# Kernel optimization log

Measured on AMD Instinct MI355X. Metric: run time of the kernel, lower is better.

Reference implementation:

```python
import jax, jax.numpy as jnp
import numpy as np

B, N, D = 2, 2048, 1024
H, FD, HD = 16, 16, 64
ENC = 512
EPS = 1e-12
RD = 4.0            # sqrt(scale_dim=feature_dim=16)
RRD = 2.0           # sqrt(RD)
R2 = float(np.sqrt(2.0))


def taylor_exp(x):
    # x: [..., fd] -> [..., 1 + fd + fd*fd]
    x2 = (x[..., :, None] * x[..., None, :]).reshape(*x.shape[:-1], FD * FD) / R2
    return jnp.concatenate([jnp.ones_like(x[..., :1]), x / RRD, x2 / RD], axis=-1)


def setup_inputs() -> dict:
    key = jax.random.key(0)
    ks = jax.random.split(key, 7)
    s = 1.0 / np.sqrt(D)
    x = jax.random.normal(ks[0], (B, N, D), dtype=jnp.float32)
    Wq = jax.random.normal(ks[1], (H * FD, D), dtype=jnp.float32) * s
    Wk = jax.random.normal(ks[2], (H * FD, D), dtype=jnp.float32) * s
    Wv = jax.random.normal(ks[3], (H * HD, D), dtype=jnp.float32) * s
    Wk_enc = jax.random.normal(ks[4], (H * FD, D), dtype=jnp.float32) * s
    Wv_enc = jax.random.normal(ks[5], (H * HD, D), dtype=jnp.float32) * s
    Wout = jax.random.normal(ks[6], (D, H * HD), dtype=jnp.float32) * s
    return {"x": x, "Wq": Wq, "Wk": Wk, "Wv": Wv,
            "Wk_enc": Wk_enc, "Wv_enc": Wv_enc, "Wout": Wout}


def reference(x, Wq, Wk, Wv, Wk_enc, Wv_enc, Wout):
    b, n, _ = x.shape
    # projections -> [b, h, n, *]
    q = (x @ Wq.T).reshape(b, n, H, FD).transpose(0, 2, 1, 3)
    k = (x @ Wk.T).reshape(b, n, H, FD).transpose(0, 2, 1, 3)
    v = (x @ Wv.T).reshape(b, n, H, HD).transpose(0, 2, 1, 3)
    # encoder prefix
    x_enc = x[:, :ENC]
    k_enc = (x_enc @ Wk_enc.T).reshape(b, ENC, H, FD).transpose(0, 2, 1, 3)
    v_enc = (x_enc @ Wv_enc.T).reshape(b, ENC, H, HD).transpose(0, 2, 1, 3)
    # Taylor feature maps: fd -> 1 + fd + fd^2 = 273
    k_enc_f = taylor_exp(k_enc)
    q_f = taylor_exp(q)
    k_f = taylor_exp(k)
    # causal decoder attention (unnormalized)
    A_qk = jnp.einsum('bhnd,bhmd->bhnm', q_f, k_f)
    A_qk = jnp.tril(A_qk)
    y1 = jnp.einsum('bhnm,bhme->bhne', A_qk, v)
    # cross attention to encoder prefix
    A_qk2 = jnp.einsum('bhnd,bhmd->bhnm', q_f, k_enc_f)
    y2 = jnp.einsum('bhnm,bhme->bhne', A_qk2, v_enc)
    # shared normalizer: enc sum + causal cumsum of decoder key features
    k_state = k_enc_f.sum(axis=2, keepdims=True) + jnp.cumsum(k_f, axis=2)
    z = 1.0 / ((q_f * k_state).sum(axis=-1) + EPS)  # [b, h, n]
    out = (y1 + y2) * z[..., None]                  # [b, h, n, hd]
    out = out.transpose(0, 2, 1, 3).reshape(b, n, H * HD)
    return out @ Wout.T
```

## Files before the change

kernel.cpp:

```cpp
#include <hip/hip_runtime.h>

#define B_    2
#define N_    2048
#define H_    16
#define HD_   64
#define ENC_  512
#define FP_   288
#define CHK_  64
#define NC_   32
#define SSZ_  18720
#define C2C_  0.17677669529663687f
#define EPS_  1e-12f

using s8v   = __attribute__((ext_vector_type(8))) short;
using h8v   = __attribute__((ext_vector_type(8))) _Float16;
using f4v   = __attribute__((ext_vector_type(4))) float;
using u16x4 = __attribute__((ext_vector_type(4))) unsigned short;
typedef unsigned short ushort_t;

__device__ __forceinline__ unsigned short bfh(float x) {
    unsigned int u = __float_as_uint(x);
    return (unsigned short)((u + 0x7FFF + ((u >> 16) & 1)) >> 16);
}
__device__ __forceinline__ float bff(unsigned short h) {
    return __uint_as_float(((unsigned int)h) << 16);
}
__device__ __forceinline__ void splitf4(float4 v, u16x4& h, u16x4& l) {
    unsigned short h0 = bfh(v.x), h1 = bfh(v.y), h2 = bfh(v.z), h3 = bfh(v.w);
    h = (u16x4){h0, h1, h2, h3};
    l = (u16x4){bfh(v.x - bff(h0)), bfh(v.y - bff(h1)),
                bfh(v.z - bff(h2)), bfh(v.w - bff(h3))};
}

__device__ __forceinline__ unsigned short f16q(float x) {
    _Float16 h = (_Float16)x;
    return __builtin_bit_cast(unsigned short, h);
}
__device__ __forceinline__ float f16f(unsigned short u) {
    return (float)__builtin_bit_cast(_Float16, u);
}
__device__ __forceinline__ void splitf16(float x, unsigned short& h, unsigned short& l) {
    _Float16 hh = (_Float16)x;
    h = __builtin_bit_cast(unsigned short, hh);
    l = f16q(x - (float)hh);
}
__device__ __forceinline__ void splitf16_4(float4 v, u16x4& h, u16x4& l) {
    unsigned short h0, l0, h1, l1, h2, l2, h3, l3;
    splitf16(v.x, h0, l0); splitf16(v.y, h1, l1);
    splitf16(v.z, h2, l2); splitf16(v.w, h3, l3);
    h = (u16x4){h0, h1, h2, h3};
    l = (u16x4){l0, l1, l2, l3};
}
__device__ __forceinline__ u16x4 f16q4(float4 v) {
    return (u16x4){f16q(v.x), f16q(v.y), f16q(v.z), f16q(v.w)};
}

#define MFMA_  __builtin_amdgcn_mfma_f32_16x16x32_bf16
#define MFMAH_ __builtin_amdgcn_mfma_f32_16x16x32_f16

__device__ __forceinline__ void gld16(const void* g, void* l) {
    __builtin_amdgcn_global_load_lds(
        (const __attribute__((address_space(1))) unsigned int*)g,
        (__attribute__((address_space(3))) unsigned int*)l, 16, 0, 0);
}

__device__ __forceinline__ int xcd_swz(int b, int nwg) {
    int q = nwg >> 3, r = nwg & 7;
    int xcd = b & 7, loc = b >> 3;
    return (xcd < r ? xcd * (q + 1) : r * (q + 1) + (xcd - r) * q) + loc;
}

#define X_F4   1048576
#define W1_F4  393216
#define W2_F4  327680
#define WO_F4  262144

__global__ __launch_bounds__(256) void split_all(
    const float* __restrict__ x,
    const float* __restrict__ Wq, const float* __restrict__ Wk,
    const float* __restrict__ Wv, const float* __restrict__ Wke,
    const float* __restrict__ Wve, const float* __restrict__ Wout,
    ushort_t* __restrict__ xh, ushort_t* __restrict__ xl,
    ushort_t* __restrict__ w1, ushort_t* __restrict__ w2,
    ushort_t* __restrict__ wo)
{
    int gid = blockIdx.x * 256 + threadIdx.x;
    if (gid < X_F4) {
        float4 vv = ((const float4*)x)[gid];
        u16x4 h, l; splitf16_4(vv, h, l);
        ((u16x4*)xh)[gid] = h; ((u16x4*)xl)[gid] = l;
    } else if (gid < X_F4 + W1_F4) {
        int i = gid - X_F4;
        int row = i >> 8, c4 = i & 255;
        const float* s = (row < 256) ? Wq + (size_t)row * 1024
                       : (row < 512) ? Wk + (size_t)(row - 256) * 1024
                                     : Wv + (size_t)(row - 512) * 1024;
        ((u16x4*)w1)[i] = f16q4(*(const float4*)(s + c4 * 4));
    } else if (gid < X_F4 + W1_F4 + W2_F4) {
        int i = gid - X_F4 - W1_F4;
        int row = i >> 8, c4 = i & 255;
        const float* s = (row < 256) ? Wke + (size_t)row * 1024
                                     : Wve + (size_t)(row - 256) * 1024;
        ((u16x4*)w2)[i] = f16q4(*(const float4*)(s + c4 * 4));
    } else {
        int i = gid - X_F4 - W1_F4 - W2_F4;
        ((u16x4*)wo)[i] = f16q4(((const float4*)Wout)[i]);
    }
}

template <int SHIFT, int PASSES>
__device__ __forceinline__ void bg128(
    const ushort_t* __restrict__ Ah, const ushort_t* __restrict__ Al,
    const ushort_t* __restrict__ Wh,
    int bx, int by, int rowjump,
    ushort_t* SM, f4v (&acc)[4][4])
{
    int t = threadIdx.x;
    int w = t >> 6, lane = t & 63;
    int row0 = by * 128, col0 = bx * 128;
    int wrow = (w >> 1) * 64, wcol = (w & 1) * 64;
    int fr = lane & 15, g = lane >> 4;

    int c0 = lane, c1 = 64 + lane;
    int r0 = w * 32 + (c0 >> 2), k80 = (c0 & 3) * 8;
    int r1 = w * 32 + (c1 >> 2), k81 = (c1 & 3) * 8;
    int gr0 = row0 + r0, gr1 = row0 + r1;
    size_t a0 = (size_t)(gr0 >> SHIFT) * rowjump + (gr0 & ((1 << SHIFT) - 1));
    size_t a1 = (size_t)(gr1 >> SHIFT) * rowjump + (gr1 & ((1 << SHIFT) - 1));
    const ushort_t* pA0h = Ah + a0 * 1024 + k80;
    const ushort_t* pA1h = Ah + a1 * 1024 + k81;
    const ushort_t* pA0l = Al + a0 * 1024 + k80;
    const ushort_t* pA1l = Al + a1 * 1024 + k81;
    const ushort_t* pW0  = Wh + (size_t)(col0 + r0) * 1024 + k80;
    const ushort_t* pW1  = Wh + (size_t)(col0 + r1) * 1024 + k81;
    int woff = w * 1024;

    #pragma unroll
    for (int mt = 0; mt < 4; ++mt)
        #pragma unroll
        for (int nt = 0; nt < 4; ++nt) acc[mt][nt] = (f4v){0.f, 0.f, 0.f, 0.f};

    auto STAGE = [&](int buf, int k0) {
        ushort_t* Bp = SM + buf * 12288;
        gld16(pA0h + k0, Bp + woff);
        gld16(pA1h + k0, Bp + woff + 512);
        if (PASSES == 2) {
            gld16(pA0l + k0, Bp + 4096 + woff);
            gld16(pA1l + k0, Bp + 4096 + woff + 512);
        }
        gld16(pW0  + k0, Bp + 8192 + woff);
        gld16(pW1  + k0, Bp + 8192 + woff + 512);
    };

    STAGE(0, 0);
    __syncthreads();
    int cur = 0;
    for (int k0 = 0; k0 < 1024; k0 += 32) {
        if (k0 + 32 < 1024) STAGE(cur ^ 1, k0 + 32);
        ushort_t* Bp = SM + cur * 12288;
        h8v a_h[4], a_l[4], b_[4];
        #pragma unroll
        for (int mt = 0; mt < 4; ++mt) {
            a_h[mt] = *(const h8v*)&Bp[(wrow + mt * 16 + fr) * 32 + g * 8];
            if (PASSES == 2)
                a_l[mt] = *(const h8v*)&Bp[4096 + (wrow + mt * 16 + fr) * 32 + g * 8];
        }
        #pragma unroll
        for (int nt = 0; nt < 4; ++nt)
            b_[nt] = *(const h8v*)&Bp[8192 + (wcol + nt * 16 + fr) * 32 + g * 8];
        #pragma unroll
        for (int mt = 0; mt < 4; ++mt)
            #pragma unroll
            for (int nt = 0; nt < 4; ++nt) {
                acc[mt][nt] = MFMAH_(a_h[mt], b_[nt], acc[mt][nt], 0, 0, 0);
                if (PASSES == 2)
                    acc[mt][nt] = MFMAH_(a_l[mt], b_[nt], acc[mt][nt], 0, 0, 0);
            }
        __syncthreads();
        cur ^= 1;
    }
}

__global__ __launch_bounds__(256) void proj2(
    const ushort_t* __restrict__ xh, const ushort_t* __restrict__ xl,
    const ushort_t* __restrict__ w1, const ushort_t* __restrict__ w2,
    float* __restrict__ tmpq, float* __restrict__ tmpk, float* __restrict__ v,
    float* __restrict__ tmpke, float* __restrict__ ve)
{
    __shared__ ushort_t SM[24576];
    f4v acc[4][4];
    int blk = xcd_swz(blockIdx.x, 464);
    int t = threadIdx.x, w = t >> 6, lane = t & 63;
    int wrow = (w >> 1) * 64, wcol = (w & 1) * 64;
    int fr = lane & 15, g = lane >> 4;

    if (blk < 384) {
        int bx = blk % 12, by = blk / 12;
        if (bx < 4) bg128<12, 2>(xh, xl, w1, bx, by, 0, SM, acc);
        else        bg128<12, 1>(xh, xl, w1, bx, by, 0, SM, acc);
        int row0 = by * 128, col0 = bx * 128;
        #pragma unroll
        for (int mt = 0; mt < 4; ++mt)
            #pragma unroll
            for (int nt = 0; nt < 4; ++nt)
                #pragma unroll
                for (int r4 = 0; r4 < 4; ++r4) {
                    int r  = row0 + wrow + mt * 16 + g * 4 + r4;
                    int cc = col0 + wcol + nt * 16 + fr;
                    float val = acc[mt][nt][r4];
                    if (cc < 256)      tmpq[(size_t)r * 256 + cc] = val;
                    else if (cc < 512) tmpk[(size_t)r * 256 + (cc - 256)] = val;
                    else {
                        int c2 = cc - 512, hh = c2 >> 6, jj = c2 & 63;
                        int bb = r >> 11, n = r & 2047;
                        v[(((size_t)(bb * 16 + hh)) * 2048 + n) * 64 + jj] = val;
                    }
                }
    } else {
        int r2 = blk - 384;
        int bx = r2 % 10, by = r2 / 10;
        if (bx < 2) bg128<9, 2>(xh, xl, w2, bx, by, 2048, SM, acc);
        else        bg128<9, 1>(xh, xl, w2, bx, by, 2048, SM, acc);
        int row0 = by * 128, col0 = bx * 128;
        #pragma unroll
        for (int mt = 0; mt < 4; ++mt)
            #pragma unroll
            for (int nt = 0; nt < 4; ++nt)
                #pragma unroll
                for (int r4 = 0; r4 < 4; ++r4) {
                    int r  = row0 + wrow + mt * 16 + g * 4 + r4;
                    int cc = col0 + wcol + nt * 16 + fr;
                    float val = acc[mt][nt][r4];
                    if (cc < 256) tmpke[(size_t)r * 256 + cc] = val;
                    else {
                        int c2 = cc - 256, hh = c2 >> 6, jj = c2 & 63;
                        int bb = r >> 9, n = r & 511;
                        ve[(((size_t)(bb * 16 + hh)) * 512 + n) * 64 + jj] = val;
                    }
                }
    }
}

__global__ __launch_bounds__(256) void out_gemm(
    const ushort_t* __restrict__ Atn, const ushort_t* __restrict__ Wh,
    float* __restrict__ out)
{
    __shared__ ushort_t SM[24576];
    f4v acc[4][4];
    int blk = xcd_swz(blockIdx.x, 256);
    int bx = blk & 7, by = blk >> 3;
    bg128<12, 1>(Atn, Atn, Wh, bx, by, 0, SM, acc);
    int t = threadIdx.x, w = t >> 6, lane = t & 63;
    int wrow = (w >> 1) * 64, wcol = (w & 1) * 64;
    int fr = lane & 15, g = lane >> 4;
    int row0 = by * 128, col0 = bx * 128;
    #pragma unroll
    for (int mt = 0; mt < 4; ++mt)
        #pragma unroll
        for (int nt = 0; nt < 4; ++nt)
            #pragma unroll
            for (int r4 = 0; r4 < 4; ++r4) {
                int r  = row0 + wrow + mt * 16 + g * 4 + r4;
                int cc = col0 + wcol + nt * 16 + fr;
                out[(size_t)r * 1024 + cc] = acc[mt][nt][r4];
            }
}

__device__ __forceinline__ void st_stage(
    const float* __restrict__ Kp, const float* __restrict__ V,
    size_t krow0, size_t vrow0, int h, int t,
    float* ksT, ushort_t* VTH)
{
    {
        int r = t >> 2, q4 = t & 3;
        float4 kv = *(const float4*)&Kp[(krow0 + r) * 256 + h * 16 + q4 * 4];
        ksT[(q4 * 4 + 0) * 68 + r] = kv.x;
        ksT[(q4 * 4 + 1) * 68 + r] = kv.y;
        ksT[(q4 * 4 + 2) * 68 + r] = kv.z;
        ksT[(q4 * 4 + 3) * 68 + r] = kv.w;
    }
    if (t < 64) ksT[16 * 68 + t] = 1.0f;
    {
        int r = t & 63, jg = t >> 6;
        #pragma unroll
        for (int cc = 0; cc < 4; ++cc) {
            float4 vv = *(const float4*)&V[(vrow0 + r) * HD_ + jg * 16 + cc * 4];
            float vals[4] = {vv.x, vv.y, vv.z, vv.w};
            #pragma unroll
            for (int e = 0; e < 4; ++e) {
                int j = jg * 16 + cc * 4 + e;
                VTH[j * 72 + r] = f16q(vals[e]);
            }
        }
    }
    if (t < 64) VTH[64 * 72 + t] = 0x3C00;
}

__device__ __forceinline__ void st_ftile(
    const float* ksT, int ft, int fr, int g,
    const h8v (&AHf)[2][5], f4v (&acc)[5])
{
    int f = ft * 16 + fr;
    int fi, fj; float scale;
    if (f == 0)       { fi = 16; fj = 16; scale = 1.0f; }
    else if (f < 17)  { fi = f - 1; fj = 16; scale = 0.5f; }
    else if (f < 273) { fi = (f - 17) >> 4; fj = (f - 17) & 15; scale = C2C_; }
    else              { fi = 16; fj = 16; scale = 0.0f; }
    #pragma unroll
    for (int ks2 = 0; ks2 < 2; ++ks2) {
        const float* pa = ksT + fi * 68 + ks2 * 32 + g * 8;
        const float* pb = ksT + fj * 68 + ks2 * 32 + g * 8;
        h8v bv;
        #pragma unroll
        for (int e = 0; e < 8; ++e) bv[e] = (_Float16)(pa[e] * pb[e] * scale);
        #pragma unroll
        for (int jt = 0; jt < 5; ++jt)
            acc[jt] = MFMAH_(AHf[ks2][jt], bv, acc[jt], 0, 0, 0);
    }
}

__global__ __launch_bounds__(256) void state_all(
    const float* __restrict__ Kpe, const float* __restrict__ Ve, ushort_t* __restrict__ Se,
    const float* __restrict__ Kpc, const float* __restrict__ Vc, ushort_t* __restrict__ Sc)
{
    __shared__ float ksT[17 * 68];
    __shared__ ushort_t VTH[80 * 72];
    int blk = blockIdx.x, t = threadIdx.x;
    int w = t >> 6, lane = t & 63, fr = lane & 15, g = lane >> 4;

    for (int i = t; i < 15 * 72; i += 256) VTH[65 * 72 + i] = 0;

    if (blk >= 160) {
        int b2 = blk - 160;
        int c = b2 & 31, bh = b2 >> 5;
        int b = bh >> 4, h = bh & 15;
        ushort_t* Sg = Sc + ((size_t)bh * NC_ + c) * SSZ_;
        st_stage(Kpc, Vc, (size_t)b * 2048 + c * 64, (size_t)bh * 2048 + c * 64,
                 h, t, ksT, VTH);
        __syncthreads();
        h8v AHf[2][5];
        #pragma unroll
        for (int ks2 = 0; ks2 < 2; ++ks2)
            #pragma unroll
            for (int jt = 0; jt < 5; ++jt)
                AHf[ks2][jt] = *(const h8v*)&VTH[(jt * 16 + fr) * 72 + ks2 * 32 + g * 8];
        for (int ft = w; ft < 18; ft += 4) {
            f4v acc[5];
            #pragma unroll
            for (int jt = 0; jt < 5; ++jt) acc[jt] = (f4v){0.f, 0.f, 0.f, 0.f};
            st_ftile(ksT, ft, fr, g, AHf, acc);
            #pragma unroll
            for (int jt = 0; jt < 5; ++jt)
                #pragma unroll
                for (int r4 = 0; r4 < 4; ++r4) {
                    int j = jt * 16 + g * 4 + r4;
                    if (j < 65) Sg[(size_t)j * FP_ + ft * 16 + fr] = f16q(acc[jt][r4]);
                }
        }
    } else {
        int bh = blk / 5, fg = blk % 5;
        int b = bh >> 4, h = bh & 15;
        int ft = fg * 4 + w;
        ushort_t* Sg = Se + (size_t)bh * SSZ_;
        f4v acc[5];
        #pragma unroll
        for (int jt = 0; jt < 5; ++jt) acc[jt] = (f4v){0.f, 0.f, 0.f, 0.f};
        for (int m0 = 0; m0 < 512; m0 += 64) {
            if (m0) __syncthreads();
            st_stage(Kpe, Ve, (size_t)b * 512 + m0, (size_t)bh * 512 + m0,
                     h, t, ksT, VTH);
            __syncthreads();
            if (ft < 18) {
                h8v AHf[2][5];
                #pragma unroll
                for (int ks2 = 0; ks2 < 2; ++ks2)
                    #pragma unroll
                    for (int jt = 0; jt < 5; ++jt)
                        AHf[ks2][jt] = *(const h8v*)&VTH[(jt * 16 + fr) * 72 + ks2 * 32 + g * 8];
                st_ftile(ksT, ft, fr, g, AHf, acc);
            }
        }
        if (ft < 18) {
            #pragma unroll
            for (int jt = 0; jt < 5; ++jt)
                #pragma unroll
                for (int r4 = 0; r4 < 4; ++r4) {
                    int j = jt * 16 + g * 4 + r4;
                    if (j < 65) Sg[(size_t)j * FP_ + ft * 16 + fr] = f16q(acc[jt][r4]);
                }
        }
    }
}

__global__ __launch_bounds__(256) void prefix_scan(
    ushort_t* __restrict__ Sloc, const ushort_t* __restrict__ Senc)
{
    const int Q = SSZ_ / 8;
    int gid = blockIdx.x * 256 + threadIdx.x;
    if (gid >= 32 * Q) return;
    int bh = gid / Q, e = gid - bh * Q;
    s8v ev = *(const s8v*)(Senc + (size_t)bh * SSZ_ + e * 8);
    float run[8];
    #pragma unroll
    for (int u = 0; u < 8; ++u) run[u] = f16f((ushort_t)ev[u]);
    ushort_t* Sb = Sloc + (size_t)bh * NC_ * SSZ_ + e * 8;
    #pragma unroll 1
    for (int cb = 0; cb < 8; ++cb) {
        s8v t0 = *(const s8v*)(Sb + (size_t)(cb * 4 + 0) * SSZ_);
        s8v t1 = *(const s8v*)(Sb + (size_t)(cb * 4 + 1) * SSZ_);
        s8v t2 = *(const s8v*)(Sb + (size_t)(cb * 4 + 2) * SSZ_);
        s8v t3 = *(const s8v*)(Sb + (size_t)(cb * 4 + 3) * SSZ_);
        s8v o0, o1, o2, o3;
        #pragma unroll
        for (int u = 0; u < 8; ++u) { o0[u] = (short)f16q(run[u]); run[u] += f16f((ushort_t)t0[u]); }
        #pragma unroll
        for (int u = 0; u < 8; ++u) { o1[u] = (short)f16q(run[u]); run[u] += f16f((ushort_t)t1[u]); }
        #pragma unroll
        for (int u = 0; u < 8; ++u) { o2[u] = (short)f16q(run[u]); run[u] += f16f((ushort_t)t2[u]); }
        #pragma unroll
        for (int u = 0; u < 8; ++u) { o3[u] = (short)f16q(run[u]); run[u] += f16f((ushort_t)t3[u]); }
        *(s8v*)(Sb + (size_t)(cb * 4 + 0) * SSZ_) = o0;
        *(s8v*)(Sb + (size_t)(cb * 4 + 1) * SSZ_) = o1;
        *(s8v*)(Sb + (size_t)(cb * 4 + 2) * SSZ_) = o2;
        *(s8v*)(Sb + (size_t)(cb * 4 + 3) * SSZ_) = o3;
    }
}

template<int FW>
__device__ __forceinline__ void y2_issue(
    const ushort_t* __restrict__ Sth, int f0, int t, s8v& r0, s8v& r1, s8v& r2)
{
    constexpr int NS = FW / 8;
    constexpr int TOT = 65 * NS;
    int s1 = t + 256, s2 = t + 512;
    r0 = *(const s8v*)(Sth + (size_t)(t / NS) * FP_ + f0 + (t % NS) * 8);
    if (s1 < TOT) r1 = *(const s8v*)(Sth + (size_t)(s1 / NS) * FP_ + f0 + (s1 % NS) * 8);
    if (FW == 64 && s2 < TOT) r2 = *(const s8v*)(Sth + (size_t)(s2 / NS) * FP_ + f0 + (s2 % NS) * 8);
}

template<int FW>
__device__ __forceinline__ void y2_write(
    ushort_t* STH, int t, const s8v& r0, const s8v& r1, const s8v& r2)
{
    constexpr int NS = FW / 8;
    constexpr int TOT = 65 * NS;
    int s1 = t + 256, s2 = t + 512;
    *(s8v*)&STH[(t / NS) * 72 + (t % NS) * 8] = r0;
    if (s1 < TOT) *(s8v*)&STH[(s1 / NS) * 72 + (s1 % NS) * 8] = r1;
    if (FW == 64 && s2 < TOT) *(s8v*)&STH[(s2 / NS) * 72 + (s2 % NS) * 8] = r2;
}

template<int FW>
__device__ __forceinline__ void qf_gen(int f0, const float* qs, ushort_t* QF1, int t)
{
    for (int i = t; i < 64 * FW; i += 256) {
        int row = i / FW, cc = i % FW;
        int f = f0 + cc;
        float qv;
        if (f == 0)       qv = 1.0f;
        else if (f < 17)  qv = qs[row * 20 + (f - 1)] * 0.5f;
        else if (f < 273) qv = qs[row * 20 + ((f - 17) >> 4)] * qs[row * 20 + ((f - 17) & 15)] * C2C_;
        else              qv = 0.0f;
        QF1[row * 72 + cc] = f16q(qv);
    }
}

template<int FW>
__device__ __forceinline__ void y2_mfma(
    const ushort_t* QF1, const ushort_t* STH,
    f4v (&acc)[5], int w, int fr, int g)
{
    #pragma unroll
    for (int ks2 = 0; ks2 < FW / 32; ++ks2) {
        h8v a = *(const h8v*)&QF1[(16 * w + fr) * 72 + ks2 * 32 + g * 8];
        #pragma unroll
        for (int jt = 0; jt < 5; ++jt) {
            h8v b = *(const h8v*)&STH[(jt * 16 + fr) * 72 + ks2 * 32 + g * 8];
            acc[jt] = MFMAH_(a, b, acc[jt], 0, 0, 0);
        }
    }
}

__global__ __launch_bounds__(256) void attn_chunk(
    const float* __restrict__ qp, const float* __restrict__ kp,
    const float* __restrict__ v, const ushort_t* __restrict__ Spre,
    ushort_t* __restrict__ atn)
{
    __shared__ ushort_t U[19456];
    __shared__ float qs[64 * 20];
    __shared__ float den_s[64];
    ushort_t* AH  = U;
    ushort_t* AL  = U + 4608;
    ushort_t* QH  = U + 9216;
    ushort_t* QL  = U + 11776;
    ushort_t* KH  = U + 14336;
    ushort_t* KL  = U + 16896;
    ushort_t* VTH = U + 9216;
    ushort_t* QF1 = U;
    ushort_t* STH = U + 9216;

    int bid = blockIdx.x;
    int bh = bid >> 5, c = bid & 31;
    int b = bh >> 4, h = bh & 15;
    int t = threadIdx.x;
    int w = t >> 6, lane = t & 63, fr = lane & 15, g = lane >> 4;
    int rowbase = b * N_ + c * CHK_;
    const ushort_t* Sth = Spre + ((size_t)bh * NC_ + c) * SSZ_;

    int rqk = t >> 2, q4 = t & 3;
    float4 qv = *(const float4*)&qp[(size_t)(rowbase + rqk) * 256 + h * 16 + q4 * 4];
    float4 kv = *(const float4*)&kp[(size_t)(rowbase + rqk) * 256 + h * 16 + q4 * 4];
    s8v rA0 = {}, rA1 = {}, rA2 = {};
    y2_issue<64>(Sth, 0, t, rA0, rA1, rA2);
    int mv = t & 63, jg0 = t >> 6;
    const float* vr = &v[((size_t)bh * N_ + c * CHK_ + mv) * HD_ + jg0 * 16];
    float4 rv0 = *(const float4*)(vr + 0);
    float4 rv1 = *(const float4*)(vr + 4);
    float4 rv2 = *(const float4*)(vr + 8);
    float4 rv3 = *(const float4*)(vr + 12);

    {
        u16x4 hh, ll;
        splitf4(qv, hh, ll);
        *(u16x4*)&QH[rqk * 40 + q4 * 4] = hh;
        *(u16x4*)&QL[rqk * 40 + q4 * 4] = ll;
        splitf4(kv, hh, ll);
        *(u16x4*)&KH[rqk * 40 + q4 * 4] = hh;
        *(u16x4*)&KL[rqk * 40 + q4 * 4] = ll;
        u16x4 z4 = (u16x4){0, 0, 0, 0};
        *(u16x4*)&QH[rqk * 40 + 16 + q4 * 4] = z4;
        *(u16x4*)&QL[rqk * 40 + 16 + q4 * 4] = z4;
        *(u16x4*)&KH[rqk * 40 + 16 + q4 * 4] = z4;
        *(u16x4*)&KL[rqk * 40 + 16 + q4 * 4] = z4;
        qs[rqk * 20 + q4 * 4 + 0] = qv.x;
        qs[rqk * 20 + q4 * 4 + 1] = qv.y;
        qs[rqk * 20 + q4 * 4 + 2] = qv.z;
        qs[rqk * 20 + q4 * 4 + 3] = qv.w;
    }
    __syncthreads();

    {
        s8v qh = *(const s8v*)&QH[(16 * w + fr) * 40 + g * 8];
        s8v ql = *(const s8v*)&QL[(16 * w + fr) * 40 + g * 8];
        f4v sacc[4];
        #pragma unroll
        for (int jt = 0; jt < 4; ++jt) sacc[jt] = (f4v){0.f, 0.f, 0.f, 0.f};
        #pragma unroll
        for (int jt = 0; jt < 4; ++jt) {
            s8v kh = *(const s8v*)&KH[(jt * 16 + fr) * 40 + g * 8];
            s8v kl = *(const s8v*)&KL[(jt * 16 + fr) * 40 + g * 8];
            sacc[jt] = MFMA_(qh, kh, sacc[jt], 0, 0, 0);
            sacc[jt] = MFMA_(qh, kl, sacc[jt], 0, 0, 0);
            sacc[jt] = MFMA_(ql, kh, sacc[jt], 0, 0, 0);
        }
        __syncthreads();
        #pragma unroll
        for (int jt = 0; jt < 4; ++jt)
            #pragma unroll
            for (int r4 = 0; r4 < 4; ++r4) {
                int row = 16 * w + g * 4 + r4, col = jt * 16 + fr;
                float s = sacc[jt][r4];
                float a = (row >= col) ? (fmaf(s, 0.25f, 1.0f) + s * s * 0.03125f) : 0.f;
                unsigned short hh, ll; splitf16(a, hh, ll);
                AH[row * 72 + col] = hh;
                AL[row * 72 + col] = ll;
            }
    }
    {
        int j0 = jg0 * 16;
        VTH[(j0 +  0) * 72 + mv] = f16q(rv0.x); VTH[(j0 +  1) * 72 + mv] = f16q(rv0.y);
        VTH[(j0 +  2) * 72 + mv] = f16q(rv0.z); VTH[(j0 +  3) * 72 + mv] = f16q(rv0.w);
        VTH[(j0 +  4) * 72 + mv] = f16q(rv1.x); VTH[(j0 +  5) * 72 + mv] = f16q(rv1.y);
        VTH[(j0 +  6) * 72 + mv] = f16q(rv1.z); VTH[(j0 +  7) * 72 + mv] = f16q(rv1.w);
        VTH[(j0 +  8) * 72 + mv] = f16q(rv2.x); VTH[(j0 +  9) * 72 + mv] = f16q(rv2.y);
        VTH[(j0 + 10) * 72 + mv] = f16q(rv2.z); VTH[(j0 + 11) * 72 + mv] = f16q(rv2.w);
        VTH[(j0 + 12) * 72 + mv] = f16q(rv3.x); VTH[(j0 + 13) * 72 + mv] = f16q(rv3.y);
        VTH[(j0 + 14) * 72 + mv] = f16q(rv3.z); VTH[(j0 + 15) * 72 + mv] = f16q(rv3.w);
    }
    if (t < 64) VTH[64 * 72 + t] = 0x3C00;
    for (int i = t; i < 15 * 72; i += 256) VTH[65 * 72 + i] = 0;
    __syncthreads();

    f4v acc[5];
    #pragma unroll
    for (int jt = 0; jt < 5; ++jt) acc[jt] = (f4v){0.f, 0.f, 0.f, 0.f};
    #pragma unroll
    for (int ks2 = 0; ks2 < 2; ++ks2) {
        h8v ah = *(const h8v*)&AH[(16 * w + fr) * 72 + ks2 * 32 + g * 8];
        h8v al = *(const h8v*)&AL[(16 * w + fr) * 72 + ks2 * 32 + g * 8];
        #pragma unroll
        for (int jt = 0; jt < 5; ++jt) {
            h8v b = *(const h8v*)&VTH[(jt * 16 + fr) * 72 + ks2 * 32 + g * 8];
            acc[jt] = MFMAH_(ah, b, acc[jt], 0, 0, 0);
            acc[jt] = MFMAH_(al, b, acc[jt], 0, 0, 0);
        }
    }
    __syncthreads();

    #pragma unroll
    for (int p = 0; p < 4; ++p) {
        y2_write<64>(STH, t, rA0, rA1, rA2);
        if (p < 3) y2_issue<64>(Sth, (p + 1) * 64, t, rA0, rA1, rA2);
        else       y2_issue<32>(Sth, 256,          t, rA0, rA1, rA2);
        qf_gen<64>(p * 64, qs, QF1, t);
        __syncthreads();
        y2_mfma<64>(QF1, STH, acc, w, fr, g);
        __syncthreads();
    }
    y2_write<32>(STH, t, rA0, rA1, rA2);
    qf_gen<32>(256, qs, QF1, t);
    __syncthreads();
    y2_mfma<32>(QF1, STH, acc, w, fr, g);

    if (fr == 0) {
        #pragma unroll
        for (int r4 = 0; r4 < 4; ++r4)
            den_s[16 * w + g * 4 + r4] = acc[4][r4];
    }
    __syncthreads();
    #pragma unroll
    for (int r4 = 0; r4 < 4; ++r4) {
        float z = 1.0f / (den_s[16 * w + g * 4 + r4] + EPS_);
        int row = rowbase + 16 * w + g * 4 + r4;
        #pragma unroll
        for (int jt = 0; jt < 4; ++jt) {
            float val = acc[jt][r4] * z;
            atn[(size_t)row * 1024 + h * 64 + jt * 16 + fr] = f16q(val);
        }
    }
}

extern "C" void kernel_launch(void* const* d_in, const int* in_sizes, int n_in,
                              void* d_out, int out_size, void* d_ws, size_t ws_size,
                              hipStream_t stream)
{
    const float* x    = (const float*)d_in[0];
    const float* Wq   = (const float*)d_in[1];
    const float* Wk   = (const float*)d_in[2];
    const float* Wv   = (const float*)d_in[3];
    const float* Wke  = (const float*)d_in[4];
    const float* Wve  = (const float*)d_in[5];
    const float* Wout = (const float*)d_in[6];
    float* out = (float*)d_out;
    float* ws  = (float*)d_ws;

    float* tmpq  = ws;
    float* tmpk  = tmpq  + (size_t)1048576;
    float* tmpke = tmpk  + (size_t)1048576;
    float* v     = tmpke + (size_t)262144;
    float* ve    = v     + (size_t)4194304;
    ushort_t* Sloc = (ushort_t*)(ve + 1048576);
    ushort_t* Senc = Sloc + (size_t)19169280;
    ushort_t* xh   = Senc + (size_t)599040;
    ushort_t* xl   = xh   + (size_t)4194304;
    ushort_t* wo   = xl   + (size_t)4194304;
    ushort_t* w1 = Sloc;
    ushort_t* w2 = w1 + (size_t)1572864;
    ushort_t* atn = xh;

    dim3 blk(256);

    split_all<<<7936, blk, 0, stream>>>(x, Wq, Wk, Wv, Wke, Wve, Wout,
                                        xh, xl, w1, w2, wo);
    proj2<<<464, blk, 0, stream>>>(xh, xl, w1, w2, tmpq, tmpk, v, tmpke, ve);
    state_all<<<160 + 32 * NC_, blk, 0, stream>>>(tmpke, ve, Senc, tmpk, v, Sloc);
    prefix_scan<<<293, blk, 0, stream>>>(Sloc, Senc);
    attn_chunk<<<32 * NC_, blk, 0, stream>>>(tmpq, tmpk, v, Sloc, atn);
    out_gemm<<<256, blk, 0, stream>>>(atn, wo, out);
}
```

Baseline: 120.8 us.

## Drop split-precision compensation passes and use single fp16 MFMA throughout

Removes the hi/lo split of x in the projection GEMMs, so the x-lo buffer, its staging and the second MFMA pass all go away. In the attention chunk kernel, the three-term bf16 split QK product becomes a single fp16 MFMA, and the A·V product drops its low-part pass. This cuts the associated LDS footprint, memory traffic and matrix work. Separately, the prefix scan moves from 8-wide to 4-wide vectors with twice the blocks, for more parallelism. The cost is reduced accuracy, since q/k projections and the Taylor scores now carry only fp16 precision, which may break the tolerance check.

```diff
diff --git a/kernel.cpp b/kernel.cpp
--- a/kernel.cpp
+++ b/kernel.cpp
@@ -13,25 +13,12 @@
 #define EPS_  1e-12f
 
 using s8v   = __attribute__((ext_vector_type(8))) short;
+using s4v   = __attribute__((ext_vector_type(4))) short;
 using h8v   = __attribute__((ext_vector_type(8))) _Float16;
 using f4v   = __attribute__((ext_vector_type(4))) float;
 using u16x4 = __attribute__((ext_vector_type(4))) unsigned short;
 typedef unsigned short ushort_t;
 
-__device__ __forceinline__ unsigned short bfh(float x) {
-    unsigned int u = __float_as_uint(x);
-    return (unsigned short)((u + 0x7FFF + ((u >> 16) & 1)) >> 16);
-}
-__device__ __forceinline__ float bff(unsigned short h) {
-    return __uint_as_float(((unsigned int)h) << 16);
-}
-__device__ __forceinline__ void splitf4(float4 v, u16x4& h, u16x4& l) {
-    unsigned short h0 = bfh(v.x), h1 = bfh(v.y), h2 = bfh(v.z), h3 = bfh(v.w);
-    h = (u16x4){h0, h1, h2, h3};
-    l = (u16x4){bfh(v.x - bff(h0)), bfh(v.y - bff(h1)),
-                bfh(v.z - bff(h2)), bfh(v.w - bff(h3))};
-}
-
 __device__ __forceinline__ unsigned short f16q(float x) {
     _Float16 h = (_Float16)x;
     return __builtin_bit_cast(unsigned short, h);
@@ -39,23 +26,10 @@
 __device__ __forceinline__ float f16f(unsigned short u) {
     return (float)__builtin_bit_cast(_Float16, u);
 }
-__device__ __forceinline__ void splitf16(float x, unsigned short& h, unsigned short& l) {
-    _Float16 hh = (_Float16)x;
-    h = __builtin_bit_cast(unsigned short, hh);
-    l = f16q(x - (float)hh);
-}
-__device__ __forceinline__ void splitf16_4(float4 v, u16x4& h, u16x4& l) {
-    unsigned short h0, l0, h1, l1, h2, l2, h3, l3;
-    splitf16(v.x, h0, l0); splitf16(v.y, h1, l1);
-    splitf16(v.z, h2, l2); splitf16(v.w, h3, l3);
-    h = (u16x4){h0, h1, h2, h3};
-    l = (u16x4){l0, l1, l2, l3};
-}
 __device__ __forceinline__ u16x4 f16q4(float4 v) {
     return (u16x4){f16q(v.x), f16q(v.y), f16q(v.z), f16q(v.w)};
 }
 
-#define MFMA_  __builtin_amdgcn_mfma_f32_16x16x32_bf16
 #define MFMAH_ __builtin_amdgcn_mfma_f32_16x16x32_f16
 
 __device__ __forceinline__ void gld16(const void* g, void* l) {
@@ -80,15 +54,13 @@
     const float* __restrict__ Wq, const float* __restrict__ Wk,
     const float* __restrict__ Wv, const float* __restrict__ Wke,
     const float* __restrict__ Wve, const float* __restrict__ Wout,
-    ushort_t* __restrict__ xh, ushort_t* __restrict__ xl,
+    ushort_t* __restrict__ xh,
     ushort_t* __restrict__ w1, ushort_t* __restrict__ w2,
     ushort_t* __restrict__ wo)
 {
     int gid = blockIdx.x * 256 + threadIdx.x;
     if (gid < X_F4) {
-        float4 vv = ((const float4*)x)[gid];
-        u16x4 h, l; splitf16_4(vv, h, l);
-        ((u16x4*)xh)[gid] = h; ((u16x4*)xl)[gid] = l;
+        ((u16x4*)xh)[gid] = f16q4(((const float4*)x)[gid]);
     } else if (gid < X_F4 + W1_F4) {
         int i = gid - X_F4;
         int row = i >> 8, c4 = i & 255;
@@ -108,10 +80,9 @@
     }
 }
 
-template <int SHIFT, int PASSES>
+template <int SHIFT>
 __device__ __forceinline__ void bg128(
-    const ushort_t* __restrict__ Ah, const ushort_t* __restrict__ Al,
-    const ushort_t* __restrict__ Wh,
+    const ushort_t* __restrict__ Ah, const ushort_t* __restrict__ Wh,
     int bx, int by, int rowjump,
     ushort_t* SM, f4v (&acc)[4][4])
 {
@@ -127,12 +98,10 @@
     int gr0 = row0 + r0, gr1 = row0 + r1;
     size_t a0 = (size_t)(gr0 >> SHIFT) * rowjump + (gr0 & ((1 << SHIFT) - 1));
     size_t a1 = (size_t)(gr1 >> SHIFT) * rowjump + (gr1 & ((1 << SHIFT) - 1));
-    const ushort_t* pA0h = Ah + a0 * 1024 + k80;
-    const ushort_t* pA1h = Ah + a1 * 1024 + k81;
-    const ushort_t* pA0l = Al + a0 * 1024 + k80;
-    const ushort_t* pA1l = Al + a1 * 1024 + k81;
-    const ushort_t* pW0  = Wh + (size_t)(col0 + r0) * 1024 + k80;
-    const ushort_t* pW1  = Wh + (size_t)(col0 + r1) * 1024 + k81;
+    const ushort_t* pA0 = Ah + a0 * 1024 + k80;
+    const ushort_t* pA1 = Ah + a1 * 1024 + k81;
+    const ushort_t* pW0 = Wh + (size_t)(col0 + r0) * 1024 + k80;
+    const ushort_t* pW1 = Wh + (size_t)(col0 + r1) * 1024 + k81;
     int woff = w * 1024;
 
     #pragma unroll
@@ -141,15 +110,11 @@
         for (int nt = 0; nt < 4; ++nt) acc[mt][nt] = (f4v){0.f, 0.f, 0.f, 0.f};
 
     auto STAGE = [&](int buf, int k0) {
-        ushort_t* Bp = SM + buf * 12288;
-        gld16(pA0h + k0, Bp + woff);
-        gld16(pA1h + k0, Bp + woff + 512);
-        if (PASSES == 2) {
-            gld16(pA0l + k0, Bp + 4096 + woff);
-            gld16(pA1l + k0, Bp + 4096 + woff + 512);
-        }
-        gld16(pW0  + k0, Bp + 8192 + woff);
-        gld16(pW1  + k0, Bp + 8192 + woff + 512);
+        ushort_t* Bp = SM + buf * 8192;
+        gld16(pA0 + k0, Bp + woff);
+        gld16(pA1 + k0, Bp + woff + 512);
+        gld16(pW0 + k0, Bp + 4096 + woff);
+        gld16(pW1 + k0, Bp + 4096 + woff + 512);
     };
 
     STAGE(0, 0);
@@ -157,37 +122,31 @@
     int cur = 0;
     for (int k0 = 0; k0 < 1024; k0 += 32) {
         if (k0 + 32 < 1024) STAGE(cur ^ 1, k0 + 32);
-        ushort_t* Bp = SM + cur * 12288;
-        h8v a_h[4], a_l[4], b_[4];
-        #pragma unroll
-        for (int mt = 0; mt < 4; ++mt) {
+        ushort_t* Bp = SM + cur * 8192;
+        h8v a_h[4], b_[4];
+        #pragma unroll
+        for (int mt = 0; mt < 4; ++mt)
             a_h[mt] = *(const h8v*)&Bp[(wrow + mt * 16 + fr) * 32 + g * 8];
-            if (PASSES == 2)
-                a_l[mt] = *(const h8v*)&Bp[4096 + (wrow + mt * 16 + fr) * 32 + g * 8];
-        }
         #pragma unroll
         for (int nt = 0; nt < 4; ++nt)
-            b_[nt] = *(const h8v*)&Bp[8192 + (wcol + nt * 16 + fr) * 32 + g * 8];
+            b_[nt] = *(const h8v*)&Bp[4096 + (wcol + nt * 16 + fr) * 32 + g * 8];
         #pragma unroll
         for (int mt = 0; mt < 4; ++mt)
             #pragma unroll
-            for (int nt = 0; nt < 4; ++nt) {
+            for (int nt = 0; nt < 4; ++nt)
                 acc[mt][nt] = MFMAH_(a_h[mt], b_[nt], acc[mt][nt], 0, 0, 0);
-                if (PASSES == 2)
-                    acc[mt][nt] = MFMAH_(a_l[mt], b_[nt], acc[mt][nt], 0, 0, 0);
-            }
         __syncthreads();
         cur ^= 1;
     }
 }
 
 __global__ __launch_bounds__(256) void proj2(
-    const ushort_t* __restrict__ xh, const ushort_t* __restrict__ xl,
+    const ushort_t* __restrict__ xh,
     const ushort_t* __restrict__ w1, const ushort_t* __restrict__ w2,
     float* __restrict__ tmpq, float* __restrict__ tmpk, float* __restrict__ v,
     float* __restrict__ tmpke, float* __restrict__ ve)
 {
-    __shared__ ushort_t SM[24576];
+    __shared__ ushort_t SM[16384];
     f4v acc[4][4];
     int blk = xcd_swz(blockIdx.x, 464);
     int t = threadIdx.x, w = t >> 6, lane = t & 63;
@@ -196,8 +155,7 @@
 
     if (blk < 384) {
         int bx = blk % 12, by = blk / 12;
-        if (bx < 4) bg128<12, 2>(xh, xl, w1, bx, by, 0, SM, acc);
-        else        bg128<12, 1>(xh, xl, w1, bx, by, 0, SM, acc);
+        bg128<12>(xh, w1, bx, by, 0, SM, acc);
         int row0 = by * 128, col0 = bx * 128;
         #pragma unroll
         for (int mt = 0; mt < 4; ++mt)
@@ -219,8 +177,7 @@
     } else {
         int r2 = blk - 384;
         int bx = r2 % 10, by = r2 / 10;
-        if (bx < 2) bg128<9, 2>(xh, xl, w2, bx, by, 2048, SM, acc);
-        else        bg128<9, 1>(xh, xl, w2, bx, by, 2048, SM, acc);
+        bg128<9>(xh, w2, bx, by, 2048, SM, acc);
         int row0 = by * 128, col0 = bx * 128;
         #pragma unroll
         for (int mt = 0; mt < 4; ++mt)
@@ -245,11 +202,11 @@
     const ushort_t* __restrict__ Atn, const ushort_t* __restrict__ Wh,
     float* __restrict__ out)
 {
-    __shared__ ushort_t SM[24576];
+    __shared__ ushort_t SM[16384];
     f4v acc[4][4];
     int blk = xcd_swz(blockIdx.x, 256);
     int bx = blk & 7, by = blk >> 3;
-    bg128<12, 1>(Atn, Atn, Wh, bx, by, 0, SM, acc);
+    bg128<12>(Atn, Wh, bx, by, 0, SM, acc);
     int t = threadIdx.x, w = t >> 6, lane = t & 63;
     int wrow = (w >> 1) * 64, wcol = (w & 1) * 64;
     int fr = lane & 15, g = lane >> 4;
@@ -395,34 +352,34 @@
 __global__ __launch_bounds__(256) void prefix_scan(
     ushort_t* __restrict__ Sloc, const ushort_t* __restrict__ Senc)
 {
-    const int Q = SSZ_ / 8;
+    const int Q = SSZ_ / 4;
     int gid = blockIdx.x * 256 + threadIdx.x;
     if (gid >= 32 * Q) return;
     int bh = gid / Q, e = gid - bh * Q;
-    s8v ev = *(const s8v*)(Senc + (size_t)bh * SSZ_ + e * 8);
-    float run[8];
-    #pragma unroll
-    for (int u = 0; u < 8; ++u) run[u] = f16f((ushort_t)ev[u]);
-    ushort_t* Sb = Sloc + (size_t)bh * NC_ * SSZ_ + e * 8;
+    s4v ev = *(const s4v*)(Senc + (size_t)bh * SSZ_ + e * 4);
+    float run[4];
+    #pragma unroll
+    for (int u = 0; u < 4; ++u) run[u] = f16f((ushort_t)ev[u]);
+    ushort_t* Sb = Sloc + (size_t)bh * NC_ * SSZ_ + e * 4;
     #pragma unroll 1
     for (int cb = 0; cb < 8; ++cb) {
-        s8v t0 = *(const s8v*)(Sb + (size_t)(cb * 4 + 0) * SSZ_);
-        s8v t1 = *(const s8v*)(Sb + (size_t)(cb * 4 + 1) * SSZ_);
-        s8v t2 = *(const s8v*)(Sb + (size_t)(cb * 4 + 2) * SSZ_);
-        s8v t3 = *(const s8v*)(Sb + (size_t)(cb * 4 + 3) * SSZ_);
-        s8v o0, o1, o2, o3;
-        #pragma unroll
-        for (int u = 0; u < 8; ++u) { o0[u] = (short)f16q(run[u]); run[u] += f16f((ushort_t)t0[u]); }
-        #pragma unroll
-        for (int u = 0; u < 8; ++u) { o1[u] = (short)f16q(run[u]); run[u] += f16f((ushort_t)t1[u]); }
-        #pragma unroll
-        for (int u = 0; u < 8; ++u) { o2[u] = (short)f16q(run[u]); run[u] += f16f((ushort_t)t2[u]); }
-        #pragma unroll
-        for (int u = 0; u < 8; ++u) { o3[u] = (short)f16q(run[u]); run[u] += f16f((ushort_t)t3[u]); }
-        *(s8v*)(Sb + (size_t)(cb * 4 + 0) * SSZ_) = o0;
-        *(s8v*)(Sb + (size_t)(cb * 4 + 1) * SSZ_) = o1;
-        *(s8v*)(Sb + (size_t)(cb * 4 + 2) * SSZ_) = o2;
-        *(s8v*)(Sb + (size_t)(cb * 4 + 3) * SSZ_) = o3;
+        s4v t0 = *(const s4v*)(Sb + (size_t)(cb * 4 + 0) * SSZ_);
+        s4v t1 = *(const s4v*)(Sb + (size_t)(cb * 4 + 1) * SSZ_);
+        s4v t2 = *(const s4v*)(Sb + (size_t)(cb * 4 + 2) * SSZ_);
+        s4v t3 = *(const s4v*)(Sb + (size_t)(cb * 4 + 3) * SSZ_);
+        s4v o0, o1, o2, o3;
+        #pragma unroll
+        for (int u = 0; u < 4; ++u) { o0[u] = (short)f16q(run[u]); run[u] += f16f((ushort_t)t0[u]); }
+        #pragma unroll
+        for (int u = 0; u < 4; ++u) { o1[u] = (short)f16q(run[u]); run[u] += f16f((ushort_t)t1[u]); }
+        #pragma unroll
+        for (int u = 0; u < 4; ++u) { o2[u] = (short)f16q(run[u]); run[u] += f16f((ushort_t)t2[u]); }
+        #pragma unroll
+        for (int u = 0; u < 4; ++u) { o3[u] = (short)f16q(run[u]); run[u] += f16f((ushort_t)t3[u]); }
+        *(s4v*)(Sb + (size_t)(cb * 4 + 0) * SSZ_) = o0;
+        *(s4v*)(Sb + (size_t)(cb * 4 + 1) * SSZ_) = o1;
+        *(s4v*)(Sb + (size_t)(cb * 4 + 2) * SSZ_) = o2;
+        *(s4v*)(Sb + (size_t)(cb * 4 + 3) * SSZ_) = o3;
     }
 }
 
@@ -486,15 +443,12 @@
     const float* __restrict__ v, const ushort_t* __restrict__ Spre,
     ushort_t* __restrict__ atn)
 {
-    __shared__ ushort_t U[19456];
+    __shared__ ushort_t U[14976];
     __shared__ float qs[64 * 20];
     __shared__ float den_s[64];
     ushort_t* AH  = U;
-    ushort_t* AL  = U + 4608;
     ushort_t* QH  = U + 9216;
-    ushort_t* QL  = U + 11776;
-    ushort_t* KH  = U + 14336;
-    ushort_t* KL  = U + 16896;
+    ushort_t* KH  = U + 11776;
     ushort_t* VTH = U + 9216;
     ushort_t* QF1 = U;
     ushort_t* STH = U + 9216;
@@ -520,18 +474,11 @@
     float4 rv3 = *(const float4*)(vr + 12);
 
     {
-        u16x4 hh, ll;
-        splitf4(qv, hh, ll);
-        *(u16x4*)&QH[rqk * 40 + q4 * 4] = hh;
-        *(u16x4*)&QL[rqk * 40 + q4 * 4] = ll;
-        splitf4(kv, hh, ll);
-        *(u16x4*)&KH[rqk * 40 + q4 * 4] = hh;
-        *(u16x4*)&KL[rqk * 40 + q4 * 4] = ll;
+        *(u16x4*)&QH[rqk * 40 + q4 * 4] = f16q4(qv);
+        *(u16x4*)&KH[rqk * 40 + q4 * 4] = f16q4(kv);
         u16x4 z4 = (u16x4){0, 0, 0, 0};
         *(u16x4*)&QH[rqk * 40 + 16 + q4 * 4] = z4;
-        *(u16x4*)&QL[rqk * 40 + 16 + q4 * 4] = z4;
         *(u16x4*)&KH[rqk * 40 + 16 + q4 * 4] = z4;
-        *(u16x4*)&KL[rqk * 40 + 16 + q4 * 4] = z4;
         qs[rqk * 20 + q4 * 4 + 0] = qv.x;
         qs[rqk * 20 + q4 * 4 + 1] = qv.y;
         qs[rqk * 20 + q4 * 4 + 2] = qv.z;
@@ -540,18 +487,14 @@
     __syncthreads();
 
     {
-        s8v qh = *(const s8v*)&QH[(16 * w + fr) * 40 + g * 8];
-        s8v ql = *(const s8v*)&QL[(16 * w + fr) * 40 + g * 8];
+        h8v qh = *(const h8v*)&QH[(16 * w + fr) * 40 + g * 8];
         f4v sacc[4];
         #pragma unroll
         for (int jt = 0; jt < 4; ++jt) sacc[jt] = (f4v){0.f, 0.f, 0.f, 0.f};
         #pragma unroll
         for (int jt = 0; jt < 4; ++jt) {
-            s8v kh = *(const s8v*)&KH[(jt * 16 + fr) * 40 + g * 8];
-            s8v kl = *(const s8v*)&KL[(jt * 16 + fr) * 40 + g * 8];
-            sacc[jt] = MFMA_(qh, kh, sacc[jt], 0, 0, 0);
-            sacc[jt] = MFMA_(qh, kl, sacc[jt], 0, 0, 0);
-            sacc[jt] = MFMA_(ql, kh, sacc[jt], 0, 0, 0);
+            h8v kh = *(const h8v*)&KH[(jt * 16 + fr) * 40 + g * 8];
+            sacc[jt] = MFMAH_(qh, kh, sacc[jt], 0, 0, 0);
         }
         __syncthreads();
         #pragma unroll
@@ -561,9 +504,7 @@
                 int row = 16 * w + g * 4 + r4, col = jt * 16 + fr;
                 float s = sacc[jt][r4];
                 float a = (row >= col) ? (fmaf(s, 0.25f, 1.0f) + s * s * 0.03125f) : 0.f;
-                unsigned short hh, ll; splitf16(a, hh, ll);
-                AH[row * 72 + col] = hh;
-                AL[row * 72 + col] = ll;
+                AH[row * 72 + col] = f16q(a);
             }
     }
     {
@@ -587,12 +528,10 @@
     #pragma unroll
     for (int ks2 = 0; ks2 < 2; ++ks2) {
         h8v ah = *(const h8v*)&AH[(16 * w + fr) * 72 + ks2 * 32 + g * 8];
-        h8v al = *(const h8v*)&AL[(16 * w + fr) * 72 + ks2 * 32 + g * 8];
         #pragma unroll
         for (int jt = 0; jt < 5; ++jt) {
             h8v b = *(const h8v*)&VTH[(jt * 16 + fr) * 72 + ks2 * 32 + g * 8];
             acc[jt] = MFMAH_(ah, b, acc[jt], 0, 0, 0);
-            acc[jt] = MFMAH_(al, b, acc[jt], 0, 0, 0);
         }
     }
     __syncthreads();
@@ -652,8 +591,7 @@
     ushort_t* Sloc = (ushort_t*)(ve + 1048576);
     ushort_t* Senc = Sloc + (size_t)19169280;
     ushort_t* xh   = Senc + (size_t)599040;
-    ushort_t* xl   = xh   + (size_t)4194304;
-    ushort_t* wo   = xl   + (size_t)4194304;
+    ushort_t* wo   = xh   + (size_t)4194304;
     ushort_t* w1 = Sloc;
     ushort_t* w2 = w1 + (size_t)1572864;
     ushort_t* atn = xh;
@@ -661,10 +599,10 @@
     dim3 blk(256);
 
     split_all<<<7936, blk, 0, stream>>>(x, Wq, Wk, Wv, Wke, Wve, Wout,
-                                        xh, xl, w1, w2, wo);
-    proj2<<<464, blk, 0, stream>>>(xh, xl, w1, w2, tmpq, tmpk, v, tmpke, ve);
+                                        xh, w1, w2, wo);
+    proj2<<<464, blk, 0, stream>>>(xh, w1, w2, tmpq, tmpk, v, tmpke, ve);
     state_all<<<160 + 32 * NC_, blk, 0, stream>>>(tmpke, ve, Senc, tmpk, v, Sloc);
-    prefix_scan<<<293, blk, 0, stream>>>(Sloc, Senc);
+    prefix_scan<<<585, blk, 0, stream>>>(Sloc, Senc);
     attn_chunk<<<32 * NC_, blk, 0, stream>>>(tmpq, tmpk, v, Sloc, atn);
     out_gemm<<<256, blk, 0, stream>>>(atn, wo, out);
 }
```

Result: faster. 109.9 us (-9.0%).
